# Optimization experiments

Hardware: AMD Instinct MI355X
Metric: run time of the kernel (lower is better)

Reference implementation:

```python
import jax, jax.numpy as jnp
import numpy as np

T, B, E, H = 4096, 2, 1024, 16          # seq, batch, embed, heads
W = 256                                  # one-sided attention window (attention_window=512 // 2)
G = 64                                   # number of global tokens (first G positions)
D = E // H
NEG = -1e9


def _band_mask():
    # valid key position for band slot j at query t is t - W + j in [0, T)
    pos = jnp.arange(T)[:, None] - W + jnp.arange(2 * W + 1)[None, :]
    return (pos >= 0) & (pos < T)  # [T, 2W+1]


def _chunk_blocks(x):
    # x: [b, t, h, d] -> key/value blocks [b, nc, 3w, h, d]; block c covers positions [c*w - w, c*w + 2w)
    b, t, h, d = x.shape
    nc = t // W
    xp = jnp.pad(x, ((0, 0), (W, 2 * W), (0, 0), (0, 0)))
    idx = jnp.arange(nc)[:, None] * W + jnp.arange(3 * W)[None, :]
    return xp[:, idx]


def _band_qk(q, k):
    # q,k: [b,t,h,d] -> banded scores [b,t,h,2w+1] (Longformer sliding_chunks_matmul_qk)
    b, t, h, d = q.shape
    nc = t // W
    qc = q.reshape(b, nc, W, h, d)
    kb = _chunk_blocks(k)
    scores = jnp.einsum('bcxhd,bcyhd->bhcxy', qc, kb)          # y in [0, 3w)
    y_idx = jnp.arange(W)[:, None] + jnp.arange(2 * W + 1)[None, :]  # [w, 2w+1]
    band = jnp.take_along_axis(scores, y_idx[None, None, None], axis=-1)
    band = band.reshape(b, h, t, 2 * W + 1).transpose(0, 2, 1, 3)
    return jnp.where(_band_mask()[None, :, None, :], band, NEG)


def _band_pv(p, v):
    # p: [b,t,h,2w+1], v: [b,t,h,d] -> [b,t,h,d] (sliding_chunks_matmul_pv)
    b, t, h, _ = p.shape
    nc = t // W
    pb = p.transpose(0, 2, 1, 3).reshape(b, h, nc, W, 2 * W + 1)
    x = jnp.arange(W)
    y_idx = x[:, None] + jnp.arange(2 * W + 1)[None, :]
    p3 = jnp.zeros((b, h, nc, W, 3 * W), p.dtype).at[:, :, :, x[:, None], y_idx].set(pb)
    vb = _chunk_blocks(v)
    out = jnp.einsum('bhcxy,bcyhd->bcxhd', p3, vb)
    return out.reshape(b, t, h, -1)


def setup_inputs() -> dict:
    key = jax.random.key(0)
    ks = jax.random.split(key, 16)
    s = 0.02
    inp = {
        'query': jax.random.normal(ks[0], (T, B, E), jnp.float32),
        'attn_mask': jnp.concatenate([jnp.ones((B, G), jnp.int64), jnp.zeros((B, T - G), jnp.int64)], axis=1),
        'Wq': jax.random.normal(ks[1], (E, E), jnp.float32) * s, 'bq': jnp.zeros((E,), jnp.float32),
        'Wk': jax.random.normal(ks[2], (E, E), jnp.float32) * s, 'bk': jnp.zeros((E,), jnp.float32),
        'Wv': jax.random.normal(ks[3], (E, E), jnp.float32) * s, 'bv': jnp.zeros((E,), jnp.float32),
        'Wqg': jax.random.normal(ks[4], (E, E), jnp.float32) * s, 'bqg': jnp.zeros((E,), jnp.float32),
        'Wkg': jax.random.normal(ks[5], (E, E), jnp.float32) * s, 'bkg': jnp.zeros((E,), jnp.float32),
        'Wvg': jax.random.normal(ks[6], (E, E), jnp.float32) * s, 'bvg': jnp.zeros((E,), jnp.float32),
        'Wo': jax.random.normal(ks[7], (E, E), jnp.float32) * s, 'bo': jnp.zeros((E,), jnp.float32),
    }
    return inp


def reference(query, attn_mask, Wq, bq, Wk, bk, Wv, bv, Wqg, bqg, Wkg, bkg, Wvg, bvg, Wo, bo):
    del attn_mask  # structure fixed: first G tokens are global, no padding
    scaling = D ** -0.5
    x = query.transpose(1, 0, 2)                      # [b, t, e]
    q = ((x @ Wq.T + bq) * scaling).reshape(B, T, H, D)
    k = (x @ Wk.T + bk).reshape(B, T, H, D)
    v = (x @ Wv.T + bv).reshape(B, T, H, D)

    band = _band_qk(q, k)                             # [b,t,h,2w+1]
    sel_w = jnp.einsum('blhd,bshd->blhs', q, k[:, :G])  # every token attends global keys
    aw = jnp.concatenate([sel_w, band], axis=-1)
    probs = jax.nn.softmax(aw.astype(jnp.float32), axis=-1).astype(aw.dtype)

    attn = jnp.einsum('blhs,bshd->blhd', probs[..., :G], v[:, :G])
    attn = attn + _band_pv(probs[..., G:], v)         # [b,t,h,d]

    # global tokens attend everything with the *_global projections
    qg = ((x[:, :G] @ Wqg.T + bqg) * scaling).reshape(B, G, H, D)
    kg = (x @ Wkg.T + bkg).reshape(B, T, H, D)
    vg = (x @ Wvg.T + bvg).reshape(B, T, H, D)
    gs = jnp.einsum('bghd,bthd->bhgt', qg, kg)
    gp = jax.nn.softmax(gs.astype(jnp.float32), axis=-1).astype(gs.dtype)
    gout = jnp.einsum('bhgt,bthd->bghd', gp, vg)
    attn = attn.at[:, :G].set(gout)

    out = attn.reshape(B, T, E).transpose(1, 0, 2) @ Wo.T + bo  # [t, b, e]
    return out
```

## Files before the change

kernel.cpp:

```cpp
#include <hip/hip_runtime.h>
#include <hip/hip_bf16.h>

typedef unsigned short u16;
typedef __bf16 bf16x8 __attribute__((ext_vector_type(8)));
typedef float  f32x4  __attribute__((ext_vector_type(4)));

constexpr int TT = 4096;
constexpr int BBATCH = 2;
constexpr int EE = 1024;
constexpr int HH = 16;
constexpr int DD = 64;
constexpr int WQ = 256;
constexpr int GG = 64;
constexpr int NSPLIT = 8;

__device__ __forceinline__ u16 f2bf(float f) {
    union { float f; unsigned int i; } c; c.f = f;
    unsigned int x = c.i;
    return (u16)((x + 0x7fffu + ((x >> 16) & 1u)) >> 16);
}
__device__ __forceinline__ uint4 pack8(float4 a, float4 b) {
    uint4 r;
    r.x = (unsigned)f2bf(a.x) | ((unsigned)f2bf(a.y) << 16);
    r.y = (unsigned)f2bf(a.z) | ((unsigned)f2bf(a.w) << 16);
    r.z = (unsigned)f2bf(b.x) | ((unsigned)f2bf(b.y) << 16);
    r.w = (unsigned)f2bf(b.z) | ((unsigned)f2bf(b.w) << 16);
    return r;
}

__device__ __forceinline__ void g2l16(const u16* g, u16* l) {
    __builtin_amdgcn_global_load_lds(
        (const __attribute__((address_space(1))) void*)g,
        (__attribute__((address_space(3))) void*)l, 16, 0, 0);
}

__device__ __forceinline__ void xcd_swizzle(int& bx, int& by) {
    bx = blockIdx.x; by = blockIdx.y;
    if ((gridDim.y & 7) == 0) {
        const int g   = blockIdx.x + blockIdx.y * gridDim.x;
        const int idx = g >> 3;
        bx = idx % gridDim.x;
        by = (g & 7) + ((idx / gridDim.x) << 3);
    }
}

struct WPtrs { const float* p[7]; };
__global__ __launch_bounds__(256) void conv_kernel(
    WPtrs wp, const float* __restrict__ query, u16* __restrict__ wb, u16* __restrict__ xb)
{
    const size_t i8 = ((size_t)blockIdx.x * 256 + threadIdx.x) << 3;
    const size_t WTOT = (size_t)7 << 20;
    const float* src;
    u16* dst;
    if (i8 < WTOT) {
        const int which = (int)(i8 >> 20);
        src = wp.p[which] + (i8 & (((size_t)1 << 20) - 1));
        dst = wb + i8;
    } else {
        const size_t j = i8 - WTOT;
        const size_t e = j & (EE - 1);
        const size_t t = (j >> 10) & (TT - 1);
        const size_t b = j >> 22;
        src = query + (t * BBATCH + b) * EE + e;
        dst = xb + j;
    }
    const float4 f0 = *(const float4*)src;
    const float4 f1 = *(const float4*)(src + 4);
    *(uint4*)dst = pack8(f0, f1);
}

template<int C_F32, int PERMA_QG, int PERMC_TB>
__global__ __launch_bounds__(256) void gemm_kernel(
    const u16* __restrict__ A, const u16* __restrict__ W, const float* __restrict__ bias,
    void* __restrict__ Cv, float scale)
{
    const int tid = threadIdx.x, lane = tid & 63, w = tid >> 6;
    const int wm = w >> 1, wn = w & 1;
    int bx, by;
    xcd_swizzle(bx, by);
    const int m0 = by << 7, n0 = bx << 7;

    __shared__ __align__(16) u16 As[2 * 128 * 32];
    __shared__ __align__(16) u16 Bs[2 * 128 * 32];

    const int lrow = lane >> 2;
    const int lcol = (lane & 3) << 3;
    auto arow = [](int m) -> size_t {
        return PERMA_QG ? (size_t)(((m >> 6) << 12) | (m & 63)) : (size_t)m;
    };
    const u16* gA0 = A + arow(m0 + (w << 4) + lrow) * EE + lcol;
    const u16* gA1 = A + arow(m0 + 64 + (w << 4) + lrow) * EE + lcol;
    const u16* gB0 = W + (size_t)(n0 + (w << 4) + lrow) * EE + lcol;
    const u16* gB1 = gB0 + (size_t)64 * EE;
    u16* lA0 = As + (w << 9);
    u16* lA1 = As + 2048 + (w << 9);
    u16* lB0 = Bs + (w << 9);
    u16* lB1 = Bs + 2048 + (w << 9);

    f32x4 acc[4][4];
#pragma unroll
    for (int i = 0; i < 4; i++)
#pragma unroll
        for (int j = 0; j < 4; j++)
            acc[i][j] = (f32x4){0.f, 0.f, 0.f, 0.f};

    const int fr = lane & 15;
    const int fq = (lane >> 4) << 3;

    for (int k0 = 0; k0 < EE; k0 += 64) {
        g2l16(gA0 + k0, lA0);  g2l16(gA0 + k0 + 32, lA0 + 4096);
        g2l16(gA1 + k0, lA1);  g2l16(gA1 + k0 + 32, lA1 + 4096);
        g2l16(gB0 + k0, lB0);  g2l16(gB0 + k0 + 32, lB0 + 4096);
        g2l16(gB1 + k0, lB1);  g2l16(gB1 + k0 + 32, lB1 + 4096);
        __syncthreads();
#pragma unroll
        for (int p = 0; p < 2; p++) {
            bf16x8 af[4], bfv[4];
#pragma unroll
            for (int i = 0; i < 4; i++)
                af[i] = *(const bf16x8*)&As[p * 4096 + ((wm << 6) + (i << 4) + fr) * 32 + fq];
#pragma unroll
            for (int j = 0; j < 4; j++)
                bfv[j] = *(const bf16x8*)&Bs[p * 4096 + ((wn << 6) + (j << 4) + fr) * 32 + fq];
#pragma unroll
            for (int i = 0; i < 4; i++)
#pragma unroll
                for (int j = 0; j < 4; j++)
                    acc[i][j] = __builtin_amdgcn_mfma_f32_16x16x32_bf16(af[i], bfv[j], acc[i][j], 0, 0, 0);
        }
        __syncthreads();
    }

    const int colbase = n0 + (wn << 6);
    const int rowbase = m0 + (wm << 6) + ((lane >> 4) << 2);
#pragma unroll
    for (int j = 0; j < 4; j++) {
        const int col = colbase + (j << 4) + fr;
        const float bv = bias[col];
#pragma unroll
        for (int i = 0; i < 4; i++) {
#pragma unroll
            for (int r = 0; r < 4; r++) {
                const int row = rowbase + (i << 4) + r;
                const float val = (acc[i][j][r] + bv) * scale;
                const size_t dst = (size_t)(PERMC_TB ? (((row & (TT - 1)) << 1) | (row >> 12)) : row) * EE + col;
                if (C_F32) ((float*)Cv)[dst] = val;
                else       ((u16*)Cv)[dst]   = f2bf(val);
            }
        }
    }
}

struct FusedArgs { u16* out[3]; const float* bias[3]; float scale[3]; int vseg; };

template<int NSEG, int CF32, int PERMC>
__global__ __launch_bounds__(256, 2) void gemm_pipe_kernel(
    const u16* __restrict__ A, const u16* __restrict__ W, FusedArgs fa)
{
    const int tid = threadIdx.x, lane = tid & 63, w = tid >> 6;
    const int wm = w >> 1, wn = w & 1;
    int bx, by;
    xcd_swizzle(bx, by);
    const int m0 = by << 7, n0 = bx << 7;

    __shared__ __align__(16) u16 As[2][8192];
    __shared__ __align__(16) u16 Bs[2][8192];

    const int srow = lane >> 3;
    const int scol = ((lane & 7) ^ srow) << 3;
    const u16* gA = A + (size_t)(m0 + (w << 5) + srow) * EE + scol;
    const u16* gB = W + (size_t)(n0 + (w << 5) + srow) * EE + scol;
    u16* lA = &As[0][0] + (w << 11);
    u16* lB = &Bs[0][0] + (w << 11);

    f32x4 acc[4][4];
#pragma unroll
    for (int i = 0; i < 4; i++)
#pragma unroll
        for (int j = 0; j < 4; j++)
            acc[i][j] = (f32x4){0.f, 0.f, 0.f, 0.f};

    const int fr = lane & 15;
    const int qb = (lane >> 4) << 4;
    const int xr = (fr & 7) << 4;

    auto stageA = [&](int k0, int buf) {
#pragma unroll
        for (int l = 0; l < 4; l++)
            g2l16(gA + (size_t)(l << 3) * EE + k0, lA + buf * 8192 + (l << 9));
    };
    auto stageB = [&](int k0, int buf) {
#pragma unroll
        for (int l = 0; l < 4; l++)
            g2l16(gB + (size_t)(l << 3) * EE + k0, lB + buf * 8192 + (l << 9));
    };

    stageA(0, 0);
    stageB(0, 0);
    __syncthreads();

    constexpr int NT = EE / 64;
#pragma unroll 2
    for (int t = 0; t < NT; t++) {
        const int buf = t & 1;
        const bool pf = (t + 1 < NT);
        const int kn = (t + 1) << 6;
        bf16x8 af[4], bfv[4];

#pragma unroll
        for (int mi = 0; mi < 4; mi++)
            af[mi] = *(const bf16x8*)((const char*)&As[buf][0] +
                      ((((wm << 6) + (mi << 4) + fr)) << 7) + (qb ^ xr));
#pragma unroll
        for (int nj = 0; nj < 4; nj++)
            bfv[nj] = *(const bf16x8*)((const char*)&Bs[buf][0] +
                      ((((wn << 6) + (nj << 4) + fr)) << 7) + (qb ^ xr));
        if (pf) stageA(kn, buf ^ 1);
        __builtin_amdgcn_s_barrier();
        __builtin_amdgcn_s_setprio(1);
#pragma unroll
        for (int mi = 0; mi < 4; mi++)
#pragma unroll
            for (int nj = 0; nj < 4; nj++)
                acc[mi][nj] = __builtin_amdgcn_mfma_f32_16x16x32_bf16(af[mi], bfv[nj], acc[mi][nj], 0, 0, 0);
        __builtin_amdgcn_s_setprio(0);
        __builtin_amdgcn_s_barrier();

#pragma unroll
        for (int mi = 0; mi < 4; mi++)
            af[mi] = *(const bf16x8*)((const char*)&As[buf][0] +
                      ((((wm << 6) + (mi << 4) + fr)) << 7) + ((64 | qb) ^ xr));
#pragma unroll
        for (int nj = 0; nj < 4; nj++)
            bfv[nj] = *(const bf16x8*)((const char*)&Bs[buf][0] +
                      ((((wn << 6) + (nj << 4) + fr)) << 7) + ((64 | qb) ^ xr));
        if (pf) stageB(kn, buf ^ 1);
        __builtin_amdgcn_s_barrier();
        __builtin_amdgcn_s_setprio(1);
#pragma unroll
        for (int mi = 0; mi < 4; mi++)
#pragma unroll
            for (int nj = 0; nj < 4; nj++)
                acc[mi][nj] = __builtin_amdgcn_mfma_f32_16x16x32_bf16(af[mi], bfv[nj], acc[mi][nj], 0, 0, 0);
        __builtin_amdgcn_s_setprio(0);
        __syncthreads();
    }

    const int seg = (NSEG > 1) ? (n0 >> 10) : 0;
    u16* outp = fa.out[seg];
    const float* bp = fa.bias[seg];
    const float scl = fa.scale[seg];
    const bool vtr = (NSEG > 1) && (seg == fa.vseg);

    const int colbase = n0 + (wn << 6);
    const int rowbase = m0 + (wm << 6) + ((lane >> 4) << 2);
#pragma unroll
    for (int j = 0; j < 4; j++) {
        const int col = colbase + (j << 4) + fr;
        const int cl  = col & (EE - 1);
        const float bv = bp[cl];
#pragma unroll
        for (int i = 0; i < 4; i++) {
            if (vtr) {
                const int row0 = rowbase + (i << 4);
                const int bb = row0 >> 12, t = row0 & (TT - 1);
                const int hh = cl >> 6, d = cl & 63;
                ushort4 pk;
                pk.x = f2bf((acc[i][j][0] + bv) * scl);
                pk.y = f2bf((acc[i][j][1] + bv) * scl);
                pk.z = f2bf((acc[i][j][2] + bv) * scl);
                pk.w = f2bf((acc[i][j][3] + bv) * scl);
                *(ushort4*)(outp + (((size_t)(bb * HH + hh) * DD + d) * TT + t)) = pk;
            } else {
#pragma unroll
                for (int r = 0; r < 4; r++) {
                    const int row = rowbase + (i << 4) + r;
                    const float val = (acc[i][j][r] + bv) * scl;
                    const size_t drow = PERMC ? (size_t)(((row & (TT - 1)) << 1) | (row >> 12))
                                              : (size_t)row;
                    if (CF32) ((float*)outp)[drow * EE + cl] = val;
                    else      outp[drow * EE + cl] = f2bf(val);
                }
            }
        }
    }
}

__global__ __launch_bounds__(256) void band_attn_kernel(
    const u16* __restrict__ q, const u16* __restrict__ k, const u16* __restrict__ vt,
    u16* __restrict__ attnb)
{
    const int tid  = threadIdx.x;
    const int lane = tid & 63;
    const int w    = tid >> 6;
    const int col  = lane & 15;
    const int quad = lane >> 4;

    const int qt = blockIdx.x >> 5;
    const int bh = blockIdx.x & 31;
    const int h  = bh & (HH - 1);
    const int b  = bh >> 4;
    const int t0 = qt << 6;

    __shared__ __align__(16) u16 Ks[64][72];
    __shared__ __align__(16) u16 Vs[64][72];
    __shared__ __align__(16) u16 Ps[4][16][72];

    const size_t base   = (size_t)b * TT * EE + (size_t)h * DD;
    const size_t vtbase = (size_t)bh * DD * TT;

    const u16* qp = q + base + (size_t)(t0 + (w << 4) + col) * EE + (quad << 3);
    const bf16x8 qf0 = *(const bf16x8*)qp;
    const bf16x8 qf1 = *(const bf16x8*)(qp + 32);

    float m_i[4], l_i[4];
    f32x4 acc_o[4];
#pragma unroll
    for (int r = 0; r < 4; r++) { m_i[r] = -1e30f; l_i[r] = 0.f; }
#pragma unroll
    for (int nt = 0; nt < 4; nt++) acc_o[nt] = (f32x4){0.f, 0.f, 0.f, 0.f};

    const int c_lo = 1 + ((t0 < WQ) ? ((WQ - t0) >> 6) : 0);
    const int c_hi = min(9, 1 + ((TT + WQ - 64 - t0) >> 6));

    const int srow  = tid >> 2;
    const int spart = (tid & 3) << 4;

    auto process = [&](int kpos0, int jbase) {
        {
            const u16* ks = k + base + (size_t)(kpos0 + srow) * EE + spart;
            const u16* vs = vt + vtbase + (size_t)srow * TT + kpos0 + spart;
            const uint4 k0v = *(const uint4*)ks;
            const uint4 k1v = *(const uint4*)(ks + 8);
            const uint4 v0v = *(const uint4*)vs;
            const uint4 v1v = *(const uint4*)(vs + 8);
            *(uint4*)&Ks[srow][spart]     = k0v;
            *(uint4*)&Ks[srow][spart + 8] = k1v;
            *(uint4*)&Vs[srow][spart]     = v0v;
            *(uint4*)&Vs[srow][spart + 8] = v1v;
        }
        __syncthreads();

        f32x4 acc_s[4];
#pragma unroll
        for (int nt = 0; nt < 4; nt++) {
            const bf16x8 kf0 = *(const bf16x8*)&Ks[(nt << 4) + col][quad << 3];
            const bf16x8 kf1 = *(const bf16x8*)&Ks[(nt << 4) + col][32 + (quad << 3)];
            f32x4 s = (f32x4){0.f, 0.f, 0.f, 0.f};
            s = __builtin_amdgcn_mfma_f32_16x16x32_bf16(qf0, kf0, s, 0, 0, 0);
            s = __builtin_amdgcn_mfma_f32_16x16x32_bf16(qf1, kf1, s, 0, 0, 0);
            acc_s[nt] = s;
        }

        if (jbase >= 0) {
#pragma unroll
            for (int nt = 0; nt < 4; nt++) {
#pragma unroll
                for (int r = 0; r < 4; r++) {
                    const int jp   = jbase + (nt << 4) + col;
                    const int qrow = (w << 4) + (quad << 2) + r;
                    const bool ok  = (jp >= qrow) && (jp <= qrow + 2 * WQ);
                    if (!ok) acc_s[nt][r] = -1e30f;
                }
            }
        }

        float p_sum[4];
#pragma unroll
        for (int r = 0; r < 4; r++) {
            float mx = fmaxf(fmaxf(acc_s[0][r], acc_s[1][r]), fmaxf(acc_s[2][r], acc_s[3][r]));
#pragma unroll
            for (int off = 1; off < 16; off <<= 1) mx = fmaxf(mx, __shfl_xor(mx, off));
            const float m_new = fmaxf(m_i[r], mx);
            const float alpha = __expf(m_i[r] - m_new);
            m_i[r] = m_new;
            l_i[r] *= alpha;
#pragma unroll
            for (int nt = 0; nt < 4; nt++) acc_o[nt][r] *= alpha;
            float ps = 0.f;
#pragma unroll
            for (int nt = 0; nt < 4; nt++) {
                const float e = __expf(acc_s[nt][r] - m_new);
                acc_s[nt][r] = e;
                ps += e;
            }
            p_sum[r] = ps;
        }
#pragma unroll
        for (int r = 0; r < 4; r++) {
            float ps = p_sum[r];
#pragma unroll
            for (int off = 1; off < 16; off <<= 1) ps += __shfl_xor(ps, off);
            l_i[r] += ps;
        }

#pragma unroll
        for (int nt = 0; nt < 4; nt++)
#pragma unroll
            for (int r = 0; r < 4; r++)
                Ps[w][(quad << 2) + r][(nt << 4) + col] = f2bf(acc_s[nt][r]);

        const bf16x8 pf0 = *(const bf16x8*)&Ps[w][col][quad << 3];
        const bf16x8 pf1 = *(const bf16x8*)&Ps[w][col][32 + (quad << 3)];

#pragma unroll
        for (int nt = 0; nt < 4; nt++) {
            const bf16x8 vf0 = *(const bf16x8*)&Vs[(nt << 4) + col][quad << 3];
            const bf16x8 vf1 = *(const bf16x8*)&Vs[(nt << 4) + col][32 + (quad << 3)];
            acc_o[nt] = __builtin_amdgcn_mfma_f32_16x16x32_bf16(pf0, vf0, acc_o[nt], 0, 0, 0);
            acc_o[nt] = __builtin_amdgcn_mfma_f32_16x16x32_bf16(pf1, vf1, acc_o[nt], 0, 0, 0);
        }
        __syncthreads();
    };

    process(0, -1);
#pragma unroll 1
    for (int c = c_lo; c <= c_hi; c++) {
        const int kpos0 = t0 - WQ + ((c - 1) << 6);
        const bool edge = (c == 1) || (c == 9);
        process(kpos0, edge ? ((c - 1) << 6) : -1);
    }

    float inv[4];
#pragma unroll
    for (int r = 0; r < 4; r++) inv[r] = 1.f / l_i[r];
#pragma unroll
    for (int nt = 0; nt < 4; nt++) {
#pragma unroll
        for (int r = 0; r < 4; r++) {
            const int t = t0 + (w << 4) + (quad << 2) + r;
            attnb[base + (size_t)t * EE + (nt << 4) + col] = f2bf(acc_o[nt][r] * inv[r]);
        }
    }
}

__global__ __launch_bounds__(256) void global_attn_flash_kernel(
    const u16* __restrict__ qg, const u16* __restrict__ kg, const u16* __restrict__ vg,
    float* __restrict__ Op, float* __restrict__ Ml, float* __restrict__ Ll)
{
    const int tid  = threadIdx.x;
    const int lane = tid & 63;
    const int w    = tid >> 6;
    const int col  = lane & 15;
    const int quad = lane >> 4;

    const int s  = blockIdx.x & (NSPLIT - 1);
    const int h  = (blockIdx.x >> 3) & (HH - 1);
    const int b  = blockIdx.x >> 7;
    const int k0pos = s * (TT / NSPLIT);

    __shared__ __align__(16) u16 Qs[64][72];
    __shared__ __align__(16) u16 Ks[64][72];
    __shared__ __align__(16) u16 Vs[64][70];
    __shared__ __align__(16) u16 Ps[4][16][72];

    const size_t base = (size_t)b * TT * EE + (size_t)h * DD;

    {
        const int qr   = tid >> 2;
        const int part = (tid & 3) << 4;
        const uint4* src = (const uint4*)(qg + (size_t)(b * GG + qr) * EE + (size_t)h * DD + part);
        *(uint4*)&Qs[qr][part]     = src[0];
        *(uint4*)&Qs[qr][part + 8] = src[1];
    }

    float m_i[4], l_i[4];
    f32x4 acc_o[4];
#pragma unroll
    for (int r = 0; r < 4; r++) { m_i[r] = -1e30f; l_i[r] = 0.f; }
#pragma unroll
    for (int nt = 0; nt < 4; nt++) acc_o[nt] = (f32x4){0.f, 0.f, 0.f, 0.f};

#pragma unroll 1
    for (int cc = 0; cc < TT / NSPLIT / 64; cc++) {
        {
            const int kk   = tid >> 2;
            const int part = (tid & 3) << 4;
            const int pos  = k0pos + (cc << 6) + kk;
            const uint4* ks = (const uint4*)(kg + base + (size_t)pos * EE + part);
            const uint4* vs = (const uint4*)(vg + base + (size_t)pos * EE + part);
            const uint4 k0v = ks[0], k1v = ks[1];
            const uint4 v0v = vs[0], v1v = vs[1];
            *(uint4*)&Ks[kk][part]     = k0v;
            *(uint4*)&Ks[kk][part + 8] = k1v;
            unsigned int* vd = (unsigned int*)&Vs[kk][part];
            vd[0] = v0v.x; vd[1] = v0v.y; vd[2] = v0v.z; vd[3] = v0v.w;
            vd[4] = v1v.x; vd[5] = v1v.y; vd[6] = v1v.z; vd[7] = v1v.w;
        }
        __syncthreads();

        bf16x8 qf0 = *(const bf16x8*)&Qs[(w << 4) + col][quad << 3];
        bf16x8 qf1 = *(const bf16x8*)&Qs[(w << 4) + col][32 + (quad << 3)];
        f32x4 acc_s[4];
#pragma unroll
        for (int nt = 0; nt < 4; nt++) {
            bf16x8 kf0 = *(const bf16x8*)&Ks[(nt << 4) + col][quad << 3];
            bf16x8 kf1 = *(const bf16x8*)&Ks[(nt << 4) + col][32 + (quad << 3)];
            f32x4 sv = (f32x4){0.f, 0.f, 0.f, 0.f};
            sv = __builtin_amdgcn_mfma_f32_16x16x32_bf16(qf0, kf0, sv, 0, 0, 0);
            sv = __builtin_amdgcn_mfma_f32_16x16x32_bf16(qf1, kf1, sv, 0, 0, 0);
            acc_s[nt] = sv;
        }

        float m_c[4], p_sum[4];
#pragma unroll
        for (int r = 0; r < 4; r++) {
            float mx = fmaxf(fmaxf(acc_s[0][r], acc_s[1][r]), fmaxf(acc_s[2][r], acc_s[3][r]));
#pragma unroll
            for (int off = 1; off < 16; off <<= 1) mx = fmaxf(mx, __shfl_xor(mx, off));
            m_c[r] = mx;
        }
#pragma unroll
        for (int r = 0; r < 4; r++) {
            const float m_new = fmaxf(m_i[r], m_c[r]);
            const float alpha = __expf(m_i[r] - m_new);
            m_i[r] = m_new;
            l_i[r] *= alpha;
#pragma unroll
            for (int nt = 0; nt < 4; nt++) acc_o[nt][r] *= alpha;
            float ps = 0.f;
#pragma unroll
            for (int nt = 0; nt < 4; nt++) {
                const float e = __expf(acc_s[nt][r] - m_new);
                acc_s[nt][r] = e;
                ps += e;
            }
            p_sum[r] = ps;
        }
#pragma unroll
        for (int r = 0; r < 4; r++) {
            float ps = p_sum[r];
#pragma unroll
            for (int off = 1; off < 16; off <<= 1) ps += __shfl_xor(ps, off);
            l_i[r] += ps;
        }

#pragma unroll
        for (int nt = 0; nt < 4; nt++)
#pragma unroll
            for (int r = 0; r < 4; r++)
                Ps[w][(quad << 2) + r][(nt << 4) + col] = f2bf(acc_s[nt][r]);

        bf16x8 pf0 = *(const bf16x8*)&Ps[w][col][quad << 3];
        bf16x8 pf1 = *(const bf16x8*)&Ps[w][col][32 + (quad << 3)];
#pragma unroll
        for (int nt = 0; nt < 4; nt++) {
            union { bf16x8 v; u16 e[8]; } vf0, vf1;
#pragma unroll
            for (int j = 0; j < 8; j++) {
                vf0.e[j] = Vs[(quad << 3) + j][(nt << 4) + col];
                vf1.e[j] = Vs[32 + (quad << 3) + j][(nt << 4) + col];
            }
            acc_o[nt] = __builtin_amdgcn_mfma_f32_16x16x32_bf16(pf0, vf0.v, acc_o[nt], 0, 0, 0);
            acc_o[nt] = __builtin_amdgcn_mfma_f32_16x16x32_bf16(pf1, vf1.v, acc_o[nt], 0, 0, 0);
        }
        __syncthreads();
    }

    const size_t obase = (size_t)blockIdx.x * GG * DD;
#pragma unroll
    for (int nt = 0; nt < 4; nt++) {
#pragma unroll
        for (int r = 0; r < 4; r++) {
            const int row = (w << 4) + (quad << 2) + r;
            Op[obase + (size_t)row * DD + (nt << 4) + col] = acc_o[nt][r];
        }
    }
    if (col == 0) {
#pragma unroll
        for (int r = 0; r < 4; r++) {
            const int row = (w << 4) + (quad << 2) + r;
            Ml[blockIdx.x * GG + row] = m_i[r];
            Ll[blockIdx.x * GG + row] = l_i[r];
        }
    }
}

__global__ __launch_bounds__(256) void global_combine_kernel(
    const float* __restrict__ Op, const float* __restrict__ Ml, const float* __restrict__ Ll,
    u16* __restrict__ attnb)
{
    const int bh  = blockIdx.x;
    const int b   = bh >> 4;
    const int h   = bh & (HH - 1);
    const int row = threadIdx.x >> 2;
    const int d0  = (threadIdx.x & 3) << 4;

    float mv[NSPLIT];
    float m = -1e30f;
#pragma unroll
    for (int s = 0; s < NSPLIT; s++) {
        mv[s] = Ml[(bh * NSPLIT + s) * GG + row];
        m = fmaxf(m, mv[s]);
    }
    float l = 0.f;
    float sc[NSPLIT];
#pragma unroll
    for (int s = 0; s < NSPLIT; s++) {
        sc[s] = __expf(mv[s] - m);
        l += Ll[(bh * NSPLIT + s) * GG + row] * sc[s];
    }
    float o[16];
#pragma unroll
    for (int j = 0; j < 16; j++) o[j] = 0.f;
#pragma unroll
    for (int s = 0; s < NSPLIT; s++) {
        const float* src = Op + ((size_t)(bh * NSPLIT + s) * GG + row) * DD + d0;
        const float f = sc[s];
#pragma unroll
        for (int j = 0; j < 16; j += 4) {
            const float4 v4 = *(const float4*)(src + j);
            o[j + 0] = fmaf(v4.x, f, o[j + 0]);
            o[j + 1] = fmaf(v4.y, f, o[j + 1]);
            o[j + 2] = fmaf(v4.z, f, o[j + 2]);
            o[j + 3] = fmaf(v4.w, f, o[j + 3]);
        }
    }
    const float inv = 1.f / l;
    u16* dst = attnb + ((size_t)b * TT + row) * EE + (size_t)h * DD + d0;
#pragma unroll
    for (int j = 0; j < 16; j++) dst[j] = f2bf(o[j] * inv);
}

extern "C" void kernel_launch(void* const* d_in, const int* in_sizes, int n_in,
                              void* d_out, int out_size, void* d_ws, size_t ws_size,
                              hipStream_t stream)
{
    (void)in_sizes; (void)n_in; (void)out_size; (void)ws_size;
    const float* query = (const float*)d_in[0];
    const float* Wq  = (const float*)d_in[2];  const float* bq  = (const float*)d_in[3];
    const float* Wk  = (const float*)d_in[4];  const float* bk  = (const float*)d_in[5];
    const float* Wv  = (const float*)d_in[6];  const float* bv  = (const float*)d_in[7];
    const float* Wqg = (const float*)d_in[8];  const float* bqg = (const float*)d_in[9];
    const float* Wkg = (const float*)d_in[10]; const float* bkg = (const float*)d_in[11];
    const float* Wvg = (const float*)d_in[12]; const float* bvg = (const float*)d_in[13];
    const float* Wo  = (const float*)d_in[14]; const float* bo  = (const float*)d_in[15];

    const size_t nfull = (size_t)BBATCH * TT * EE;
    const size_t wsz   = (size_t)1 << 20;
    u16* xb    = (u16*)d_ws;
    u16* wb    = xb + nfull;
    u16* slotA = wb + 7 * wsz;
    u16* slotB = slotA + nfull;
    u16* slotC = slotB + nfull;
    u16* qg    = slotC + nfull;
    float* Op  = (float*)(qg + (size_t)BBATCH * GG * EE);
    float* Ml  = Op + (size_t)BBATCH * HH * NSPLIT * GG * DD;
    float* Ll  = Ml + (size_t)BBATCH * HH * NSPLIT * GG;
    u16* attnb = xb;

    WPtrs wp;
    wp.p[0] = Wq; wp.p[1] = Wk; wp.p[2] = Wv;
    wp.p[3] = Wkg; wp.p[4] = Wvg; wp.p[5] = Wqg; wp.p[6] = Wo;

    const dim3 blk(256);
    const dim3 gF2(16, 64);
    const dim3 gF3(24, 64);
    const dim3 gFull(8, 64);
    const dim3 gQg(8, 1);
    const float sc = 0.125f;

    conv_kernel<<<7680, blk, 0, stream>>>(wp, query, wb, xb);

    gemm_kernel<0, 1, 0><<<gQg, blk, 0, stream>>>(xb, wb + 5 * wsz, bqg, qg, sc);

    FusedArgs fa2;
    fa2.out[0] = slotA; fa2.out[1] = slotB; fa2.out[2] = nullptr;
    fa2.bias[0] = bkg;  fa2.bias[1] = bvg;  fa2.bias[2] = nullptr;
    fa2.scale[0] = 1.f; fa2.scale[1] = 1.f; fa2.scale[2] = 1.f;
    fa2.vseg = -1;
    gemm_pipe_kernel<2, 0, 0><<<gF2, blk, 0, stream>>>(xb, wb + 3 * wsz, fa2);
    global_attn_flash_kernel<<<BBATCH * HH * NSPLIT, blk, 0, stream>>>(qg, slotA, slotB, Op, Ml, Ll);

    FusedArgs fa3;
    fa3.out[0] = slotA; fa3.out[1] = slotB; fa3.out[2] = slotC;
    fa3.bias[0] = bq;   fa3.bias[1] = bk;   fa3.bias[2] = bv;
    fa3.scale[0] = sc;  fa3.scale[1] = 1.f; fa3.scale[2] = 1.f;
    fa3.vseg = 2;
    gemm_pipe_kernel<3, 0, 0><<<gF3, blk, 0, stream>>>(xb, wb, fa3);

    band_attn_kernel<<<BBATCH * HH * (TT / 64), blk, 0, stream>>>(slotA, slotB, slotC, attnb);
    global_combine_kernel<<<BBATCH * HH, blk, 0, stream>>>(Op, Ml, Ll, attnb);

    FusedArgs faO;
    faO.out[0] = (u16*)d_out; faO.out[1] = nullptr; faO.out[2] = nullptr;
    faO.bias[0] = bo;         faO.bias[1] = nullptr; faO.bias[2] = nullptr;
    faO.scale[0] = 1.f;       faO.scale[1] = 1.f;    faO.scale[2] = 1.f;
    faO.vseg = -1;
    gemm_pipe_kernel<1, 1, 1><<<gFull, blk, 0, stream>>>(attnb, wb + 6 * wsz, faO);
}
```

Baseline: 366.0 us.

## Double-buffer K/V tiles and transpose score MFMA in band attention

The band attention kernel now double-buffers the K/V shared-memory tiles. Next-tile global loads are issued into registers before the current tile's compute, and written to the alternate buffer afterwards, which removes one barrier per iteration and hides global load latency. The QK^T MFMA operands are swapped so each lane holds one query row's scores. That lets the row max and sum reduce with two cross-lane shuffles instead of four per row. P is packed with the hardware v_cvt_pk_bf16 instruction, at the cost of extra shuffles to redistribute alpha and l and doubled K/V LDS usage.

New measurement: 343.1 us. 6.3% less time.

```diff
diff --git a/kernel.cpp b/kernel.cpp
--- a/kernel.cpp
+++ b/kernel.cpp
@@ -18,6 +18,11 @@
     union { float f; unsigned int i; } c; c.f = f;
     unsigned int x = c.i;
     return (u16)((x + 0x7fffu + ((x >> 16) & 1u)) >> 16);
+}
+__device__ __forceinline__ unsigned cvt_pk_bf16(float a, float b) {
+    unsigned r;
+    asm("v_cvt_pk_bf16_f32 %0, %1, %2" : "=v"(r) : "v"(a), "v"(b));
+    return r;
 }
 __device__ __forceinline__ uint4 pack8(float4 a, float4 b) {
     uint4 r;
@@ -302,8 +307,8 @@
     const int b  = bh >> 4;
     const int t0 = qt << 6;
 
-    __shared__ __align__(16) u16 Ks[64][72];
-    __shared__ __align__(16) u16 Vs[64][72];
+    __shared__ __align__(16) u16 Ks[2][64][72];
+    __shared__ __align__(16) u16 Vs[2][64][72];
     __shared__ __align__(16) u16 Ps[4][16][72];
 
     const size_t base   = (size_t)b * TT * EE + (size_t)h * DD;
@@ -313,43 +318,59 @@
     const bf16x8 qf0 = *(const bf16x8*)qp;
     const bf16x8 qf1 = *(const bf16x8*)(qp + 32);
 
-    float m_i[4], l_i[4];
+    float m_i = -1e30f, l_i = 0.f;
     f32x4 acc_o[4];
-#pragma unroll
-    for (int r = 0; r < 4; r++) { m_i[r] = -1e30f; l_i[r] = 0.f; }
 #pragma unroll
     for (int nt = 0; nt < 4; nt++) acc_o[nt] = (f32x4){0.f, 0.f, 0.f, 0.f};
 
     const int c_lo = 1 + ((t0 < WQ) ? ((WQ - t0) >> 6) : 0);
     const int c_hi = min(9, 1 + ((TT + WQ - 64 - t0) >> 6));
+    const int NTL  = 2 + c_hi - c_lo;
 
     const int srow  = tid >> 2;
     const int spart = (tid & 3) << 4;
 
-    auto process = [&](int kpos0, int jbase) {
-        {
-            const u16* ks = k + base + (size_t)(kpos0 + srow) * EE + spart;
-            const u16* vs = vt + vtbase + (size_t)srow * TT + kpos0 + spart;
-            const uint4 k0v = *(const uint4*)ks;
-            const uint4 k1v = *(const uint4*)(ks + 8);
-            const uint4 v0v = *(const uint4*)vs;
-            const uint4 v1v = *(const uint4*)(vs + 8);
-            *(uint4*)&Ks[srow][spart]     = k0v;
-            *(uint4*)&Ks[srow][spart + 8] = k1v;
-            *(uint4*)&Vs[srow][spart]     = v0v;
-            *(uint4*)&Vs[srow][spart + 8] = v1v;
-        }
+    uint4 kr0, kr1, vr0, vr1;
+    auto issue_loads = [&](int i) {
+        const int kpos0 = (i == 0) ? 0 : (t0 - WQ + ((c_lo + i - 2) << 6));
+        const u16* ks = k + base + (size_t)(kpos0 + srow) * EE + spart;
+        const u16* vs = vt + vtbase + (size_t)srow * TT + kpos0 + spart;
+        kr0 = *(const uint4*)ks;
+        kr1 = *(const uint4*)(ks + 8);
+        vr0 = *(const uint4*)vs;
+        vr1 = *(const uint4*)(vs + 8);
+    };
+    auto write_stage = [&](int buf) {
+        *(uint4*)&Ks[buf][srow][spart]     = kr0;
+        *(uint4*)&Ks[buf][srow][spart + 8] = kr1;
+        *(uint4*)&Vs[buf][srow][spart]     = vr0;
+        *(uint4*)&Vs[buf][srow][spart + 8] = vr1;
+    };
+
+    issue_loads(0);
+    write_stage(0);
+    int buf = 0;
+
+    const int qrow = (w << 4) + col;
+    const int alsrc0 = (lane & 48) | ((lane >> 2) & 12);
+
+#pragma unroll 1
+    for (int i = 0; i < NTL; i++) {
         __syncthreads();
-
-        f32x4 acc_s[4];
+        const int c     = c_lo + i - 1;
+        const int jbase = (i > 0 && (c == 1 || c == 9)) ? ((c - 1) << 6) : -1;
+        const bool pf   = (i + 1 < NTL);
+        if (pf) issue_loads(i + 1);
+
+        f32x4 sT[4];
 #pragma unroll
         for (int nt = 0; nt < 4; nt++) {
-            const bf16x8 kf0 = *(const bf16x8*)&Ks[(nt << 4) + col][quad << 3];
-            const bf16x8 kf1 = *(const bf16x8*)&Ks[(nt << 4) + col][32 + (quad << 3)];
+            const bf16x8 kf0 = *(const bf16x8*)&Ks[buf][(nt << 4) + col][quad << 3];
+            const bf16x8 kf1 = *(const bf16x8*)&Ks[buf][(nt << 4) + col][32 + (quad << 3)];
             f32x4 s = (f32x4){0.f, 0.f, 0.f, 0.f};
-            s = __builtin_amdgcn_mfma_f32_16x16x32_bf16(qf0, kf0, s, 0, 0, 0);
-            s = __builtin_amdgcn_mfma_f32_16x16x32_bf16(qf1, kf1, s, 0, 0, 0);
-            acc_s[nt] = s;
+            s = __builtin_amdgcn_mfma_f32_16x16x32_bf16(kf0, qf0, s, 0, 0, 0);
+            s = __builtin_amdgcn_mfma_f32_16x16x32_bf16(kf1, qf1, s, 0, 0, 0);
+            sT[nt] = s;
         }
 
         if (jbase >= 0) {
@@ -357,73 +378,71 @@
             for (int nt = 0; nt < 4; nt++) {
 #pragma unroll
                 for (int r = 0; r < 4; r++) {
-                    const int jp   = jbase + (nt << 4) + col;
-                    const int qrow = (w << 4) + (quad << 2) + r;
-                    const bool ok  = (jp >= qrow) && (jp <= qrow + 2 * WQ);
-                    if (!ok) acc_s[nt][r] = -1e30f;
+                    const int jp = jbase + (nt << 4) + (quad << 2) + r;
+                    const bool ok = (jp >= qrow) && (jp <= qrow + 2 * WQ);
+                    if (!ok) sT[nt][r] = -1e30f;
                 }
             }
         }
 
-        float p_sum[4];
-#pragma unroll
-        for (int r = 0; r < 4; r++) {
-            float mx = fmaxf(fmaxf(acc_s[0][r], acc_s[1][r]), fmaxf(acc_s[2][r], acc_s[3][r]));
-#pragma unroll
-            for (int off = 1; off < 16; off <<= 1) mx = fmaxf(mx, __shfl_xor(mx, off));
-            const float m_new = fmaxf(m_i[r], mx);
-            const float alpha = __expf(m_i[r] - m_new);
-            m_i[r] = m_new;
-            l_i[r] *= alpha;
-#pragma unroll
-            for (int nt = 0; nt < 4; nt++) acc_o[nt][r] *= alpha;
-            float ps = 0.f;
-#pragma unroll
-            for (int nt = 0; nt < 4; nt++) {
-                const float e = __expf(acc_s[nt][r] - m_new);
-                acc_s[nt][r] = e;
+        float mx = sT[0][0];
+#pragma unroll
+        for (int nt = 0; nt < 4; nt++)
+#pragma unroll
+            for (int r = 0; r < 4; r++) mx = fmaxf(mx, sT[nt][r]);
+        mx = fmaxf(mx, __shfl_xor(mx, 16));
+        mx = fmaxf(mx, __shfl_xor(mx, 32));
+        const float m_new = fmaxf(m_i, mx);
+        const float alpha = __expf(m_i - m_new);
+        m_i = m_new;
+        l_i *= alpha;
+        float ps = 0.f;
+#pragma unroll
+        for (int nt = 0; nt < 4; nt++)
+#pragma unroll
+            for (int r = 0; r < 4; r++) {
+                const float e = __expf(sT[nt][r] - m_new);
+                sT[nt][r] = e;
                 ps += e;
             }
-            p_sum[r] = ps;
-        }
-#pragma unroll
-        for (int r = 0; r < 4; r++) {
-            float ps = p_sum[r];
-#pragma unroll
-            for (int off = 1; off < 16; off <<= 1) ps += __shfl_xor(ps, off);
-            l_i[r] += ps;
-        }
-
+        ps += __shfl_xor(ps, 16);
+        ps += __shfl_xor(ps, 32);
+        l_i += ps;
+
+        float al[4];
+#pragma unroll
+        for (int r = 0; r < 4; r++) al[r] = __shfl(alpha, alsrc0 | r);
 #pragma unroll
         for (int nt = 0; nt < 4; nt++)
 #pragma unroll
-            for (int r = 0; r < 4; r++)
-                Ps[w][(quad << 2) + r][(nt << 4) + col] = f2bf(acc_s[nt][r]);
+            for (int r = 0; r < 4; r++) acc_o[nt][r] *= al[r];
+
+#pragma unroll
+        for (int nt = 0; nt < 4; nt++) {
+            uint2 pk2;
+            pk2.x = cvt_pk_bf16(sT[nt][0], sT[nt][1]);
+            pk2.y = cvt_pk_bf16(sT[nt][2], sT[nt][3]);
+            *(uint2*)&Ps[w][col][(nt << 4) + (quad << 2)] = pk2;
+        }
 
         const bf16x8 pf0 = *(const bf16x8*)&Ps[w][col][quad << 3];
         const bf16x8 pf1 = *(const bf16x8*)&Ps[w][col][32 + (quad << 3)];
 
 #pragma unroll
         for (int nt = 0; nt < 4; nt++) {
-            const bf16x8 vf0 = *(const bf16x8*)&Vs[(nt << 4) + col][quad << 3];
-            const bf16x8 vf1 = *(const bf16x8*)&Vs[(nt << 4) + col][32 + (quad << 3)];
+            const bf16x8 vf0 = *(const bf16x8*)&Vs[buf][(nt << 4) + col][quad << 3];
+            const bf16x8 vf1 = *(const bf16x8*)&Vs[buf][(nt << 4) + col][32 + (quad << 3)];
             acc_o[nt] = __builtin_amdgcn_mfma_f32_16x16x32_bf16(pf0, vf0, acc_o[nt], 0, 0, 0);
             acc_o[nt] = __builtin_amdgcn_mfma_f32_16x16x32_bf16(pf1, vf1, acc_o[nt], 0, 0, 0);
         }
-        __syncthreads();
-    };
-
-    process(0, -1);
-#pragma unroll 1
-    for (int c = c_lo; c <= c_hi; c++) {
-        const int kpos0 = t0 - WQ + ((c - 1) << 6);
-        const bool edge = (c == 1) || (c == 9);
-        process(kpos0, edge ? ((c - 1) << 6) : -1);
+
+        if (pf) write_stage(buf ^ 1);
+        buf ^= 1;
     }
 
     float inv[4];
 #pragma unroll
-    for (int r = 0; r < 4; r++) inv[r] = 1.f / l_i[r];
+    for (int r = 0; r < 4; r++) inv[r] = 1.f / __shfl(l_i, alsrc0 | r);
 #pragma unroll
     for (int nt = 0; nt < 4; nt++) {
 #pragma unroll
```
